# Optimization experiments

Hardware: AMD Instinct MI355X
Metric: run time of the kernel (lower is better)

## Reference

```python
import jax, jax.numpy as jnp
import numpy as np

TAGSET_BASE = 48            # original tag vocabulary
T = TAGSET_BASE + 2         # + START + STOP
START, STOP = TAGSET_BASE, TAGSET_BASE + 1
B, L = 1024, 512
NEG = -10000.0


def setup_inputs() -> dict:
    key = jax.random.key(0)
    k1, k2, k3, k4 = jax.random.split(key, 4)
    logits = jax.random.normal(k1, (B, L, T), dtype=jnp.float32)
    labels = jax.random.randint(k2, (B, L), 0, TAGSET_BASE)
    lens = jax.random.randint(k3, (B,), 1, L + 1)
    transitions = jax.random.normal(k4, (T, T), dtype=jnp.float32)
    transitions = transitions.at[START, :].set(NEG).at[:, STOP].set(NEG)
    return {"logits": logits, "transitions": transitions,
            "labels": labels, "lens": lens}


def reference(logits, transitions, labels, lens):
    """CRF negative log-likelihood: mean(partition - emission - transition)."""
    Bs, Ls, Ts = logits.shape
    start, stop = Ts - 2, Ts - 1

    # ---- forward algorithm (log-partition) via scan over time ----
    alpha0 = jnp.full((Bs, Ts), NEG, dtype=logits.dtype).at[:, start].set(0.0)

    def step(carry, logit_t):  # logit_t: [B, T]
        alpha, c = carry
        # mat[b,i,j] = trans[i,j] + alpha[b,j] + logit[b,i]
        mat = transitions[None, :, :] + alpha[:, None, :] + logit_t[:, :, None]
        alpha_nxt = jax.nn.logsumexp(mat, axis=2)
        alpha = jnp.where((c > 0)[:, None], alpha_nxt, alpha)
        return (alpha, c - 1), None

    (alpha, _), _ = jax.lax.scan(step, (alpha0, lens), jnp.swapaxes(logits, 0, 1))
    partition = jax.nn.logsumexp(alpha + transitions[stop][None, :], axis=1)  # [B]

    # ---- transition score of gold path ----
    labels_ext = jnp.concatenate([
        jnp.full((Bs, 1), start, dtype=labels.dtype),
        labels,
        jnp.full((Bs, 1), stop, dtype=labels.dtype)], axis=1)      # [B, L+2]
    pos = jnp.arange(Ls + 2)
    keep = pos[None, :] < (lens + 1)[:, None]
    labels_ext = jnp.where(keep, labels_ext, stop)
    # trans[next_tag, prev_tag]
    trn_scr = transitions[labels_ext[:, 1:], labels_ext[:, :-1]]   # [B, L+1]
    tmask = (jnp.arange(Ls + 1)[None, :] < (lens + 1)[:, None]).astype(logits.dtype)
    trans_score = jnp.sum(trn_scr * tmask, axis=1)                 # [B]

    # ---- emission score of gold path ----
    em = jnp.take_along_axis(logits, labels[:, :, None], axis=2)[:, :, 0]  # [B, L]
    emask = (jnp.arange(Ls)[None, :] < lens[:, None]).astype(logits.dtype)
    emission = jnp.sum(em * emask, axis=1)                         # [B]

    return jnp.sum(partition - emission - trans_score) / Bs
```

## Files before the change

### kernel.cpp

```cpp
#include <hip/hip_runtime.h>

#define TT 50
#define START_TAG 48
#define STOP_TAG 49
#define BB 1024
#define LL 512

#define UP_THR   0x1p63f
#define DOWN_THR 0x1p-32f
#define OFF_64LN2 44.3614195558364998f

#define RING 16
#define PF   10

typedef __attribute__((address_space(3))) uint32_t lds_u32_t;
typedef __attribute__((address_space(1))) const uint32_t glb_u32_t;

__device__ __forceinline__ void load_lds4(const float* g, float* l) {
    __builtin_amdgcn_global_load_lds((glb_u32_t*)g, (lds_u32_t*)l, 4, 0, 0);
}
__device__ __forceinline__ float rdlane(uint32_t u, int j) {
    return __uint_as_float(__builtin_amdgcn_readlane(u, j));
}

template<bool BWD>
__device__ __forceinline__ void crf_step(
    float& e, float& moff, float& elg, float& lgN1,
    const float (&Mreg)[49], const float* __restrict__ gp,
    float (&ring)[RING][64], int lane, int k, int nsteps, int len, bool rescale)
{
    {
        int kk = k + PF; int cl = nsteps - 1;
        kk = (kk > cl) ? cl : kk; kk = (kk < 0) ? 0 : kk;
        int t = BWD ? (len - 1 - kk) : kk;
        load_lds4(gp + (size_t)t * TT, &ring[(k + PF) & (RING - 1)][0]);
    }

    float elgN = __expf(lgN1);

    float x = BWD ? (e * elg) : e;
    const uint32_t xu = __float_as_uint(x);
    float ebc[49];
#pragma unroll
    for (int j = 0; j < 49; ++j) {
        const int sl = BWD ? ((j < 48) ? j : 49) : j;
        ebc[j] = rdlane(xu, sl);
    }
    __builtin_amdgcn_sched_barrier(0);

    float a0 = 0.f, a1 = 0.f, a2 = 0.f, a3 = 0.f;
#pragma unroll
    for (int j = 0; j < 48; j += 4) {
        a0 = fmaf(Mreg[j + 0], ebc[j + 0], a0);
        a1 = fmaf(Mreg[j + 1], ebc[j + 1], a1);
        a2 = fmaf(Mreg[j + 2], ebc[j + 2], a2);
        a3 = fmaf(Mreg[j + 3], ebc[j + 3], a3);
    }
    a0 = fmaf(Mreg[48], ebc[48], a0);
    float s = (a0 + a1) + (a2 + a3);

    float en = BWD ? s : s * elg;
    en = (lane < TT) ? en : 0.0f;

    if (rescale) {
        if (__any(en > UP_THR))          { en *= 0x1p-64f; moff += OFF_64LN2; }
        else if (!__any(en > DOWN_THR))  { en *= 0x1p64f;  moff -= OFF_64LN2; }
    }
    e = en;

    asm volatile("s_waitcnt vmcnt(8)" ::: "memory");
    __builtin_amdgcn_sched_barrier(0);
    lgN1 = ring[(k + 2) & (RING - 1)][lane];
    elg = elgN;
}

template<bool BWD>
__device__ __forceinline__ void crf_body(
    int b, int lane,
    const float* __restrict__ logits, const float* __restrict__ trans,
    const int* __restrict__ lens,
    float* __restrict__ vec_out, float* __restrict__ scale_out,
    float (&ring)[RING][64])
{
    const int len    = lens[b];
    const int mid    = len >> 1;
    const int nsteps = BWD ? (len - mid) : mid;

    float Mreg[49];
    {
        const int lc = (lane < TT) ? lane : 0;
#pragma unroll
        for (int k = 0; k < 49; ++k) {
            const int src = BWD ? ((k < 48) ? k : 49) : k;
            float tv = BWD ? trans[src * TT + lc] : trans[lc * TT + src];
            float m = __expf(tv);
            Mreg[k] = (lane < TT) ? m : 0.0f;
        }
    }

    const int lane_c = (lane < TT) ? lane : (TT - 1);
    const float* gp = logits + (size_t)b * LL * TT + lane_c;

#pragma unroll
    for (int i = 0; i < PF; ++i) {
        int kk = i; int cl = nsteps - 1;
        kk = (kk > cl) ? cl : kk; kk = (kk < 0) ? 0 : kk;
        int t = BWD ? (len - 1 - kk) : kk;
        load_lds4(gp + (size_t)t * TT, &ring[i][0]);
    }
    asm volatile("s_waitcnt vmcnt(8)" ::: "memory");
    __builtin_amdgcn_sched_barrier(0);
    float elg  = __expf(ring[0][lane]);
    float lgN1 = ring[1][lane];

    float e = BWD ? ((lane < TT) ? __expf(trans[STOP_TAG * TT + lane]) : 0.0f)
                  : ((lane == START_TAG) ? 1.0f : 0.0f);
    float moff = 0.0f;

    int k = 0;
    for (; k + 2 <= nsteps; k += 2) {
        crf_step<BWD>(e, moff, elg, lgN1, Mreg, gp, ring, lane, k,     nsteps, len, false);
        crf_step<BWD>(e, moff, elg, lgN1, Mreg, gp, ring, lane, k + 1, nsteps, len, true);
    }
    if (k < nsteps)
        crf_step<BWD>(e, moff, elg, lgN1, Mreg, gp, ring, lane, k, nsteps, len, true);

    float mm = e;
#pragma unroll
    for (int o = 32; o > 0; o >>= 1) mm = fmaxf(mm, __shfl_xor(mm, o));
    vec_out[b * 64 + lane] = e * (1.0f / mm);
    if (lane == 0) scale_out[b] = moff + __logf(mm);
}

__global__ __launch_bounds__(64) void crf_fwdbwd(
    const float* __restrict__ logits, const float* __restrict__ trans,
    const int* __restrict__ lens,
    float* __restrict__ fvec, float* __restrict__ fs,
    float* __restrict__ bvec, float* __restrict__ bs)
{
    __shared__ __align__(16) float ring[RING][64];
    const int b   = blockIdx.x >> 1;
    const bool bw = blockIdx.x & 1;
    if (bw) crf_body<true >(b, threadIdx.x, logits, trans, lens, bvec, bs, ring);
    else    crf_body<false>(b, threadIdx.x, logits, trans, lens, fvec, fs, ring);
}

__global__ __launch_bounds__(64) void crf_scores(
    const float* __restrict__ logits,
    const float* __restrict__ trans,
    const int* __restrict__ labels,
    const int* __restrict__ lens,
    float* __restrict__ score_out)
{
    const int b    = blockIdx.x;
    const int lane = threadIdx.x;
    const int len  = lens[b];

    float acc = 0.0f;
    for (int t = lane; t < len; t += 64) {
        int lab = labels[b * LL + t];
        acc += logits[((size_t)b * LL + t) * TT + lab];
        int prev = (t == 0) ? START_TAG : labels[b * LL + t - 1];
        acc += trans[lab * TT + prev];
    }
    if (lane == 0) acc += trans[STOP_TAG * TT + labels[b * LL + (len - 1)]];

#pragma unroll
    for (int o = 32; o > 0; o >>= 1) acc += __shfl_xor(acc, o);
    if (lane == 0) score_out[b] = acc;
}

__global__ __launch_bounds__(64) void crf_combine(
    const float* __restrict__ fvec, const float* __restrict__ bvec,
    const float* __restrict__ fs,   const float* __restrict__ bs,
    const float* __restrict__ score, float* __restrict__ nll)
{
    const int b = blockIdx.x, lane = threadIdx.x;
    float p = fvec[b * 64 + lane] * bvec[b * 64 + lane];
#pragma unroll
    for (int o = 32; o > 0; o >>= 1) p += __shfl_xor(p, o);
    if (lane == 0) nll[b] = (__logf(p) + fs[b] + bs[b]) - score[b];
}

__global__ __launch_bounds__(1024) void crf_reduce(
    const float* __restrict__ nll, float* __restrict__ out)
{
    __shared__ float red[16];
    const int tid = threadIdx.x;
    float acc = nll[tid];
#pragma unroll
    for (int o = 32; o > 0; o >>= 1) acc += __shfl_xor(acc, o);
    if ((tid & 63) == 0) red[tid >> 6] = acc;
    __syncthreads();
    if (tid == 0) {
        float tot = 0.0f;
        for (int i = 0; i < 16; ++i) tot += red[i];
        out[0] = tot / (float)BB;
    }
}

extern "C" void kernel_launch(void* const* d_in, const int* in_sizes, int n_in,
                              void* d_out, int out_size, void* d_ws, size_t ws_size,
                              hipStream_t stream) {
    const float* logits = (const float*)d_in[0];
    const float* trans  = (const float*)d_in[1];
    const int*   labels = (const int*)d_in[2];
    const int*   lens   = (const int*)d_in[3];

    float* fvec  = (float*)d_ws;
    float* bvec  = fvec + BB * 64;
    float* fs    = bvec + BB * 64;
    float* bs    = fs + BB;
    float* score = bs + BB;
    float* nll   = score + BB;
    float* out   = (float*)d_out;

    crf_fwdbwd<<<2 * BB, 64, 0, stream>>>(logits, trans, lens, fvec, fs, bvec, bs);
    crf_scores<<<BB, 64, 0, stream>>>(logits, trans, labels, lens, score);
    crf_combine<<<BB, 64, 0, stream>>>(fvec, bvec, fs, bs, score, nll);
    crf_reduce<<<1, 1024, 0, stream>>>(nll, out);
}
```

Baseline: 112.1 us.

## Fuse forward, backward, scores and combine into one 3-wave block with LDS broadcast

Merges the forward and backward chains, the gold-path scoring and the combine step into a single kernel that uses three wavefronts per batch row, exchanging results through shared memory instead of workspace round-trips and extra launches. The per-step broadcast of the state vector now goes through LDS with float4 reads rather than 49 readlane operations, and the prefetch ring shrinks from 16 to 8 entries. This removes two kernel launches and global traffic. In exchange it adds an LDS write/read round-trip on every serial step, with no barrier between the write and the cross-lane reads, and a smaller prefetch distance on the latency-critical recurrence.

```diff
diff --git a/kernel.cpp b/kernel.cpp
--- a/kernel.cpp
+++ b/kernel.cpp
@@ -10,8 +10,8 @@
 #define DOWN_THR 0x1p-32f
 #define OFF_64LN2 44.3614195558364998f
 
-#define RING 16
-#define PF   10
+#define RING 8
+#define PF   8
 
 typedef __attribute__((address_space(3))) uint32_t lds_u32_t;
 typedef __attribute__((address_space(1))) const uint32_t glb_u32_t;
@@ -19,167 +19,143 @@
 __device__ __forceinline__ void load_lds4(const float* g, float* l) {
     __builtin_amdgcn_global_load_lds((glb_u32_t*)g, (lds_u32_t*)l, 4, 0, 0);
 }
-__device__ __forceinline__ float rdlane(uint32_t u, int j) {
-    return __uint_as_float(__builtin_amdgcn_readlane(u, j));
-}
 
 template<bool BWD>
-__device__ __forceinline__ void crf_step(
-    float& e, float& moff, float& elg, float& lgN1,
-    const float (&Mreg)[49], const float* __restrict__ gp,
-    float (&ring)[RING][64], int lane, int k, int nsteps, int len, bool rescale)
+__device__ __forceinline__ void run_chain(
+    int b, int lane, int len,
+    const float* __restrict__ logits, const float* __restrict__ trans,
+    float (*ring)[64], float* __restrict__ bc,
+    float& e_out, float& moff_out)
 {
-    {
-        int kk = k + PF; int cl = nsteps - 1;
-        kk = (kk > cl) ? cl : kk; kk = (kk < 0) ? 0 : kk;
-        int t = BWD ? (len - 1 - kk) : kk;
-        load_lds4(gp + (size_t)t * TT, &ring[(k + PF) & (RING - 1)][0]);
-    }
-
-    float elgN = __expf(lgN1);
-
-    float x = BWD ? (e * elg) : e;
-    const uint32_t xu = __float_as_uint(x);
-    float ebc[49];
-#pragma unroll
-    for (int j = 0; j < 49; ++j) {
-        const int sl = BWD ? ((j < 48) ? j : 49) : j;
-        ebc[j] = rdlane(xu, sl);
-    }
-    __builtin_amdgcn_sched_barrier(0);
-
-    float a0 = 0.f, a1 = 0.f, a2 = 0.f, a3 = 0.f;
-#pragma unroll
-    for (int j = 0; j < 48; j += 4) {
-        a0 = fmaf(Mreg[j + 0], ebc[j + 0], a0);
-        a1 = fmaf(Mreg[j + 1], ebc[j + 1], a1);
-        a2 = fmaf(Mreg[j + 2], ebc[j + 2], a2);
-        a3 = fmaf(Mreg[j + 3], ebc[j + 3], a3);
-    }
-    a0 = fmaf(Mreg[48], ebc[48], a0);
-    float s = (a0 + a1) + (a2 + a3);
-
-    float en = BWD ? s : s * elg;
-    en = (lane < TT) ? en : 0.0f;
-
-    if (rescale) {
-        if (__any(en > UP_THR))          { en *= 0x1p-64f; moff += OFF_64LN2; }
-        else if (!__any(en > DOWN_THR))  { en *= 0x1p64f;  moff -= OFF_64LN2; }
-    }
-    e = en;
-
-    asm volatile("s_waitcnt vmcnt(8)" ::: "memory");
-    __builtin_amdgcn_sched_barrier(0);
-    lgN1 = ring[(k + 2) & (RING - 1)][lane];
-    elg = elgN;
-}
-
-template<bool BWD>
-__device__ __forceinline__ void crf_body(
-    int b, int lane,
-    const float* __restrict__ logits, const float* __restrict__ trans,
-    const int* __restrict__ lens,
-    float* __restrict__ vec_out, float* __restrict__ scale_out,
-    float (&ring)[RING][64])
-{
-    const int len    = lens[b];
     const int mid    = len >> 1;
     const int nsteps = BWD ? (len - mid) : mid;
 
-    float Mreg[49];
+    float4 Mf[13];
     {
         const int lc = (lane < TT) ? lane : 0;
 #pragma unroll
-        for (int k = 0; k < 49; ++k) {
-            const int src = BWD ? ((k < 48) ? k : 49) : k;
-            float tv = BWD ? trans[src * TT + lc] : trans[lc * TT + src];
-            float m = __expf(tv);
-            Mreg[k] = (lane < TT) ? m : 0.0f;
+        for (int p = 0; p < 13; ++p) {
+            float mv[4];
+#pragma unroll
+            for (int q = 0; q < 4; ++q) {
+                const int j = 4 * p + q;
+                float v = 0.0f;
+                if (j < TT && lane < TT)
+                    v = __expf(BWD ? trans[j * TT + lc] : trans[lc * TT + j]);
+                mv[q] = v;
+            }
+            Mf[p] = make_float4(mv[0], mv[1], mv[2], mv[3]);
         }
     }
-
-    const int lane_c = (lane < TT) ? lane : (TT - 1);
-    const float* gp = logits + (size_t)b * LL * TT + lane_c;
-
-#pragma unroll
-    for (int i = 0; i < PF; ++i) {
-        int kk = i; int cl = nsteps - 1;
-        kk = (kk > cl) ? cl : kk; kk = (kk < 0) ? 0 : kk;
-        int t = BWD ? (len - 1 - kk) : kk;
-        load_lds4(gp + (size_t)t * TT, &ring[i][0]);
-    }
-    asm volatile("s_waitcnt vmcnt(8)" ::: "memory");
-    __builtin_amdgcn_sched_barrier(0);
-    float elg  = __expf(ring[0][lane]);
-    float lgN1 = ring[1][lane];
 
     float e = BWD ? ((lane < TT) ? __expf(trans[STOP_TAG * TT + lane]) : 0.0f)
                   : ((lane == START_TAG) ? 1.0f : 0.0f);
     float moff = 0.0f;
 
-    int k = 0;
-    for (; k + 2 <= nsteps; k += 2) {
-        crf_step<BWD>(e, moff, elg, lgN1, Mreg, gp, ring, lane, k,     nsteps, len, false);
-        crf_step<BWD>(e, moff, elg, lgN1, Mreg, gp, ring, lane, k + 1, nsteps, len, true);
+    if (nsteps > 0) {
+        const int lane_c = (lane < TT) ? lane : (TT - 1);
+        const float* gp = logits + (size_t)b * LL * TT + lane_c;
+
+#pragma unroll
+        for (int i = 0; i < PF; ++i) {
+            int kk = i; if (kk > nsteps - 1) kk = nsteps - 1;
+            int t = BWD ? (len - 1 - kk) : kk;
+            load_lds4(gp + (size_t)t * TT, &ring[i][0]);
+        }
+        asm volatile("s_waitcnt vmcnt(6)" ::: "memory");
+        __builtin_amdgcn_sched_barrier(0);
+        float elg  = __expf(ring[0][lane]);
+        float lgN1 = ring[1][lane];
+
+        for (int k = 0; k < nsteps; ++k) {
+            asm volatile("s_waitcnt vmcnt(5)" ::: "memory");
+            __builtin_amdgcn_sched_barrier(0);
+            float lgN2 = ring[(k + 2) & (RING - 1)][lane];
+            {
+                int kk = k + PF; if (kk > nsteps - 1) kk = nsteps - 1;
+                int t = BWD ? (len - 1 - kk) : kk;
+                load_lds4(gp + (size_t)t * TT, &ring[(k + PF) & (RING - 1)][0]);
+            }
+            float elgN = __expf(lgN1);
+
+            bc[lane] = BWD ? (e * elg) : e;
+
+            float4 acc = make_float4(0.f, 0.f, 0.f, 0.f);
+#pragma unroll
+            for (int p = 0; p < 13; ++p) {
+                float4 f = *reinterpret_cast<const float4*>(&bc[4 * p]);
+                acc.x = fmaf(Mf[p].x, f.x, acc.x);
+                acc.y = fmaf(Mf[p].y, f.y, acc.y);
+                acc.z = fmaf(Mf[p].z, f.z, acc.z);
+                acc.w = fmaf(Mf[p].w, f.w, acc.w);
+            }
+            float s  = (acc.x + acc.y) + (acc.z + acc.w);
+            float en = BWD ? s : s * elg;
+
+            if (k & 1) {
+                if (__any(en > UP_THR))         { en *= 0x1p-64f; moff += OFF_64LN2; }
+                else if (!__any(en > DOWN_THR)) { en *= 0x1p64f;  moff -= OFF_64LN2; }
+            }
+            e = en; elg = elgN; lgN1 = lgN2;
+        }
     }
-    if (k < nsteps)
-        crf_step<BWD>(e, moff, elg, lgN1, Mreg, gp, ring, lane, k, nsteps, len, true);
 
     float mm = e;
 #pragma unroll
     for (int o = 32; o > 0; o >>= 1) mm = fmaxf(mm, __shfl_xor(mm, o));
-    vec_out[b * 64 + lane] = e * (1.0f / mm);
-    if (lane == 0) scale_out[b] = moff + __logf(mm);
+    e_out = e * (1.0f / mm);
+    moff_out = moff + __logf(mm);
 }
 
-__global__ __launch_bounds__(64) void crf_fwdbwd(
+__global__ __launch_bounds__(192) void crf_main(
     const float* __restrict__ logits, const float* __restrict__ trans,
-    const int* __restrict__ lens,
-    float* __restrict__ fvec, float* __restrict__ fs,
-    float* __restrict__ bvec, float* __restrict__ bs)
+    const int* __restrict__ labels, const int* __restrict__ lens,
+    float* __restrict__ nll)
 {
-    __shared__ __align__(16) float ring[RING][64];
-    const int b   = blockIdx.x >> 1;
-    const bool bw = blockIdx.x & 1;
-    if (bw) crf_body<true >(b, threadIdx.x, logits, trans, lens, bvec, bs, ring);
-    else    crf_body<false>(b, threadIdx.x, logits, trans, lens, fvec, fs, ring);
-}
+    __shared__ __align__(16) float ringF[RING][64];
+    __shared__ __align__(16) float ringB[RING][64];
+    __shared__ __align__(16) float bcF[64];
+    __shared__ __align__(16) float bcB[64];
+    __shared__ __align__(16) float xchB[64];
+    __shared__ float moffB_sh, score_sh;
 
-__global__ __launch_bounds__(64) void crf_scores(
-    const float* __restrict__ logits,
-    const float* __restrict__ trans,
-    const int* __restrict__ labels,
-    const int* __restrict__ lens,
-    float* __restrict__ score_out)
-{
     const int b    = blockIdx.x;
-    const int lane = threadIdx.x;
+    const int wid  = threadIdx.x >> 6;
+    const int lane = threadIdx.x & 63;
     const int len  = lens[b];
 
-    float acc = 0.0f;
-    for (int t = lane; t < len; t += 64) {
-        int lab = labels[b * LL + t];
-        acc += logits[((size_t)b * LL + t) * TT + lab];
-        int prev = (t == 0) ? START_TAG : labels[b * LL + t - 1];
-        acc += trans[lab * TT + prev];
+    float eF = 0.0f, moffF = 0.0f;
+
+    if (wid == 0) {
+        run_chain<false>(b, lane, len, logits, trans, ringF, bcF, eF, moffF);
+    } else if (wid == 1) {
+        float eB, moffB;
+        run_chain<true>(b, lane, len, logits, trans, ringB, bcB, eB, moffB);
+        xchB[lane] = eB;
+        if (lane == 0) moffB_sh = moffB;
+    } else {
+        float acc = 0.0f;
+        for (int t = lane; t < len; t += 64) {
+            int lab = labels[b * LL + t];
+            acc += logits[((size_t)b * LL + t) * TT + lab];
+            int prev = (t == 0) ? START_TAG : labels[b * LL + t - 1];
+            acc += trans[lab * TT + prev];
+        }
+        if (lane == 0) acc += trans[STOP_TAG * TT + labels[b * LL + (len - 1)]];
+#pragma unroll
+        for (int o = 32; o > 0; o >>= 1) acc += __shfl_xor(acc, o);
+        if (lane == 0) score_sh = acc;
     }
-    if (lane == 0) acc += trans[STOP_TAG * TT + labels[b * LL + (len - 1)]];
 
+    __syncthreads();
+
+    if (wid == 0) {
+        float p = eF * xchB[lane];
 #pragma unroll
-    for (int o = 32; o > 0; o >>= 1) acc += __shfl_xor(acc, o);
-    if (lane == 0) score_out[b] = acc;
-}
-
-__global__ __launch_bounds__(64) void crf_combine(
-    const float* __restrict__ fvec, const float* __restrict__ bvec,
-    const float* __restrict__ fs,   const float* __restrict__ bs,
-    const float* __restrict__ score, float* __restrict__ nll)
-{
-    const int b = blockIdx.x, lane = threadIdx.x;
-    float p = fvec[b * 64 + lane] * bvec[b * 64 + lane];
-#pragma unroll
-    for (int o = 32; o > 0; o >>= 1) p += __shfl_xor(p, o);
-    if (lane == 0) nll[b] = (__logf(p) + fs[b] + bs[b]) - score[b];
+        for (int o = 32; o > 0; o >>= 1) p += __shfl_xor(p, o);
+        if (lane == 0)
+            nll[b] = (moffF + moffB_sh + __logf(p)) - score_sh;
+    }
 }
 
 __global__ __launch_bounds__(1024) void crf_reduce(
@@ -207,16 +183,9 @@
     const int*   labels = (const int*)d_in[2];
     const int*   lens   = (const int*)d_in[3];
 
-    float* fvec  = (float*)d_ws;
-    float* bvec  = fvec + BB * 64;
-    float* fs    = bvec + BB * 64;
-    float* bs    = fs + BB;
-    float* score = bs + BB;
-    float* nll   = score + BB;
-    float* out   = (float*)d_out;
+    float* nll = (float*)d_ws;
+    float* out = (float*)d_out;
 
-    crf_fwdbwd<<<2 * BB, 64, 0, stream>>>(logits, trans, lens, fvec, fs, bvec, bs);
-    crf_scores<<<BB, 64, 0, stream>>>(logits, trans, labels, lens, score);
-    crf_combine<<<BB, 64, 0, stream>>>(fvec, bvec, fs, bs, score, nll);
+    crf_main<<<BB, 192, 0, stream>>>(logits, trans, labels, lens, nll);
     crf_reduce<<<1, 1024, 0, stream>>>(nll, out);
 }
```

After: 146.4 us. 1.31x slower.
